# Optimization experiments

Measured on AMD Instinct MI355X. Metric: run time of the kernel, lower is better.

The kernel has to match this reference:

```python
import jax, jax.numpy as jnp
import numpy as np
from jax import lax

DROPOUT_RATE = 0.1  # config['dropout']


def setup_inputs() -> dict:
    key = jax.random.key(0)
    kx, kl, kwi, kwh = jax.random.split(key, 4)
    B, T, D, H = 64, 2048, 256, 256
    datamat = jax.random.normal(kx, (B, T, D), dtype=jnp.float32)
    datalens = jax.random.randint(kl, (B,), 1, T + 1, dtype=jnp.int32)
    # OptimizedLSTMCell params: combined input/hidden kernels, gate order (i, f, g, o)
    s_i = 1.0 / np.sqrt(D)
    s_h = 1.0 / np.sqrt(H)
    Wi = jax.random.uniform(kwi, (D, 4 * H), jnp.float32, -s_i, s_i)
    Wh = jax.random.uniform(kwh, (H, 4 * H), jnp.float32, -s_h, s_h)
    b = jnp.zeros((4 * H,), dtype=jnp.float32)
    return {"datamat": datamat, "Wi": Wi, "Wh": Wh, "b": b, "datalens": datalens}


def _dropout(x, rate):
    # training=True dropout with a fixed key (deterministic reference)
    keep = jax.random.bernoulli(jax.random.key(42), 1.0 - rate, x.shape)
    return jnp.where(keep, x / (1.0 - rate), jnp.zeros_like(x))


def _lstm_forward(x, Wi, Wh, b, datalens):
    # x: [B, T, D]
    B, T, D = x.shape
    H = Wh.shape[0]

    def step(carry, xt):
        c, h = carry
        z = xt @ Wi + h @ Wh + b  # [B, 4H], gate order i, f, g, o
        i, f, g, o = jnp.split(z, 4, axis=-1)
        c_new = jax.nn.sigmoid(f) * c + jax.nn.sigmoid(i) * jnp.tanh(g)
        h_new = jax.nn.sigmoid(o) * jnp.tanh(c_new)
        return (c_new, h_new), (c_new, h_new)

    c0 = jnp.zeros((B, H), dtype=x.dtype)
    h0 = jnp.zeros((B, H), dtype=x.dtype)
    _, (cs, hs) = lax.scan(step, (c0, h0), jnp.swapaxes(x, 0, 1))  # [T, B, H] each
    outputs = jnp.swapaxes(hs, 0, 1)  # [B, T, H]
    # flax nn.RNN with seq_lengths + return_carry: select carry at t = len-1 per batch
    idx = jnp.clip(datalens.astype(jnp.int32) - 1, 0, T - 1)  # [B]
    bidx = jnp.arange(B)
    c_last = cs[idx, bidx]  # [B, H]
    h_last = hs[idx, bidx]  # [B, H]
    return (c_last, h_last), outputs


def reference(datamat, Wi, Wh, b, datalens):
    x = _dropout(datamat, DROPOUT_RATE)
    out_carry, outputs = _lstm_forward(x, Wi, Wh, b, datalens)
    return (out_carry, outputs)
```

## Files before the change

kernel.cpp:

```cpp
#include <hip/hip_runtime.h>


typedef __attribute__((ext_vector_type(8))) short short8;
typedef __attribute__((ext_vector_type(4))) float floatx4;
typedef __attribute__((ext_vector_type(4))) int int4v;
typedef __attribute__((ext_vector_type(4))) unsigned short us4;
typedef __attribute__((ext_vector_type(2))) unsigned int uint2v;

#define LOG2E 1.44269504088896f

__device__ __forceinline__ unsigned short f2bf(float f) {
  unsigned int u = __float_as_uint(f);
  u = u + 0x7fffu + ((u >> 16) & 1u);
  return (unsigned short)(u >> 16);
}
__device__ __forceinline__ float fexp2(float x) { return __builtin_amdgcn_exp2f(x); }
__device__ __forceinline__ float frcp(float x) { return __builtin_amdgcn_rcpf(x); }

__device__ __forceinline__ unsigned int tf_bits(unsigned int x0, unsigned int x1) {
  const unsigned int K0 = 0u, K1 = 42u;
  const unsigned int KX = K0 ^ K1 ^ 0x1BD11BDAu;
  x0 += K0; x1 += K1;
#define TF_R(r) { x0 += x1; x1 = (x1 << (r)) | (x1 >> (32 - (r))); x1 ^= x0; }
  TF_R(13) TF_R(15) TF_R(26) TF_R(6)   x0 += K1; x1 += KX + 1u;
  TF_R(17) TF_R(29) TF_R(16) TF_R(24)  x0 += KX; x1 += K0 + 2u;
  TF_R(13) TF_R(15) TF_R(26) TF_R(6)   x0 += K0; x1 += K1 + 3u;
  TF_R(17) TF_R(29) TF_R(16) TF_R(24)  x0 += K1; x1 += KX + 4u;
  TF_R(13) TF_R(15) TF_R(26) TF_R(6)   x0 += KX; x1 += K0 + 5u;
#undef TF_R
  return x0 ^ x1;
}

__global__ __launch_bounds__(256) void k_dropout(const float* __restrict__ x,
                                                 unsigned short* __restrict__ xd) {
  const unsigned int base = (blockIdx.x * 256u + threadIdx.x) * 4u;
  const float4 xv = *reinterpret_cast<const float4*>(x + base);
  const float xs[4] = {xv.x, xv.y, xv.z, xv.w};
  us4 o;
#pragma unroll
  for (int j = 0; j < 4; ++j) {
    const unsigned int bits = tf_bits(0u, base + (unsigned int)j);
    const float u = __uint_as_float((bits >> 9) | 0x3f800000u) - 1.0f;
    const float v = (u < 0.9f) ? (xs[j] / 0.9f) : 0.0f;
    o[j] = f2bf(v);
  }
  *reinterpret_cast<us4*>(xd + base) = o;
}

__global__ __launch_bounds__(256) void k_pack_wi(const float* __restrict__ wi,
                                                 unsigned short* __restrict__ wit) {
  __shared__ float tile[32][33];
  const int k0 = blockIdx.x * 32, n0 = blockIdx.y * 32;
  const int tx = threadIdx.x & 31, ty = threadIdx.x >> 5;
#pragma unroll
  for (int i = 0; i < 4; ++i)
    tile[ty + i * 8][tx] = wi[(k0 + ty + i * 8) * 1024 + n0 + tx];
  __syncthreads();
#pragma unroll
  for (int i = 0; i < 4; ++i)
    wit[(n0 + ty + i * 8) * 256 + k0 + tx] = f2bf(tile[tx][ty + i * 8]);
}

__global__ __launch_bounds__(256) void k_colscale(const float* __restrict__ wh,
                                                  float* __restrict__ dq,
                                                  float* __restrict__ qs) {
  __shared__ float red[256];
  const int t = threadIdx.x;
  const int n = blockIdx.x * 16 + (t & 15);
  const int kg = t >> 4;
  float m = 0.f;
#pragma unroll
  for (int i = 0; i < 16; ++i)
    m = fmaxf(m, fabsf(wh[(kg * 16 + i) * 1024 + n]));
  red[t] = m;
  __syncthreads();
  if (t < 16) {
    const int nn = blockIdx.x * 16 + t;
    float mm = red[t];
#pragma unroll
    for (int j = 1; j < 16; ++j) mm = fmaxf(mm, red[t + j * 16]);
    const float s = (mm > 0.f) ? mm : 1.f;
    const float gsc[4] = {LOG2E, -LOG2E, 2.f * LOG2E, LOG2E};
    dq[nn] = (s / 16129.0f) * gsc[nn >> 8];
    qs[nn] = 127.0f / s;
  }
}

__global__ __launch_bounds__(256) void k_pack_wh_i8(const float* __restrict__ wh,
                                                    const float* __restrict__ qs,
                                                    signed char* __restrict__ wq) {
  const int tid = blockIdx.x * 256 + threadIdx.x;
  const int j = tid & 15, l = (tid >> 4) & 63, kt = (tid >> 10) & 3, ntg = tid >> 12;
  const int k = kt * 64 + ((l >> 4) << 4) + j;
  const int n = ntg * 16 + (l & 15);
  float v = rintf(wh[k * 1024 + n] * qs[n]);
  v = fminf(fmaxf(v, -127.f), 127.f);
  wq[tid] = (signed char)(int)v;
}

__global__ __launch_bounds__(512, 2) void k_fused(
    const unsigned short* __restrict__ xd, const unsigned short* __restrict__ wit,
    const float* __restrict__ bias, unsigned short* __restrict__ xp,
    const signed char* __restrict__ wq, const float* __restrict__ dq,
    const int* __restrict__ lens, float* __restrict__ out,
    unsigned int* __restrict__ flags) {
  __shared__ __align__(16) unsigned short SH[45056];

  const int tid = threadIdx.x, lane = tid & 63;

  if (blockIdx.x >= 32) {
    const int gb = (int)blockIdx.x - 32;
    const int tc = gb >> 9;
    const int rem = gb & 511;
    const int b = rem >> 3, y = rem & 7;
    const int m0 = b * 2048 + tc * 128;

    const int wv = tid >> 6;
    const int wm = wv >> 2;
    const int wn = wv & 3;
    const int srow = tid >> 2, sseg = tid & 3;
    const unsigned short* gA = xd + (m0 + srow) * 256 + sseg * 8;
    const int nsrc = ((srow >> 5) << 8) + y * 32 + (srow & 31);
    const unsigned short* gB = wit + nsrc * 256 + sseg * 8;
    const int soff = srow * 40 + sseg * 8;

    const floatx4 zero4 = {0.f, 0.f, 0.f, 0.f};
    floatx4 acc[4][2];
#pragma unroll
    for (int i = 0; i < 4; ++i) { acc[i][0] = zero4; acc[i][1] = zero4; }

    short8 ra = *(const short8*)(gA);
    short8 rb = *(const short8*)(gB);
    *(short8*)&SH[soff] = ra;
    *(short8*)&SH[10240 + soff] = rb;
    __syncthreads();

    const int frow = (lane & 15) * 40 + ((lane >> 4) << 3);
#pragma unroll 1
    for (int kt = 0; kt < 8; ++kt) {
      const int boff = (kt & 1) * 5120;
      if (kt < 7) {
        ra = *(const short8*)(gA + (kt + 1) * 32);
        rb = *(const short8*)(gB + (kt + 1) * 32);
      }
      short8 af[4], bfv[2];
#pragma unroll
      for (int mt = 0; mt < 4; ++mt)
        af[mt] = *(const short8*)&SH[boff + (wm * 64 + mt * 16) * 40 + frow];
#pragma unroll
      for (int nt = 0; nt < 2; ++nt)
        bfv[nt] = *(const short8*)&SH[10240 + boff + (wn * 32 + nt * 16) * 40 + frow];
#pragma unroll
      for (int mt = 0; mt < 4; ++mt)
#pragma unroll
        for (int nt = 0; nt < 2; ++nt)
          acc[mt][nt] = __builtin_amdgcn_mfma_f32_16x16x32_bf16(af[mt], bfv[nt], acc[mt][nt], 0, 0, 0);
      if (kt < 7) {
        const int noff = boff ^ 5120;
        *(short8*)&SH[noff + soff] = ra;
        *(short8*)&SH[10240 + noff + soff] = rb;
      }
      __syncthreads();
    }

    const float gsc[4] = {LOG2E, -LOG2E, 2.f * LOG2E, LOG2E};
    const float gv = gsc[wn];
    float bv[2];
#pragma unroll
    for (int nt = 0; nt < 2; ++nt)
      bv[nt] = bias[wn * 256 + y * 32 + nt * 16 + (lane & 15)];

    __syncthreads();
#pragma unroll
    for (int mt = 0; mt < 4; ++mt)
#pragma unroll
      for (int nt = 0; nt < 2; ++nt) {
        const int jj = wn * 32 + nt * 16 + (lane & 15);
#pragma unroll
        for (int q = 0; q < 4; ++q) {
          const int row = wm * 64 + mt * 16 + ((lane >> 4) << 2) + q;
          SH[row * 132 + jj] = f2bf((acc[mt][nt][q] + bv[nt]) * gv);
        }
      }
    __syncthreads();

#pragma unroll
    for (int k = 0; k < 8; ++k) {
      const int pi = k * 512 + tid;
      const int row = pi >> 5, u = pi & 31;
      us4 o = {SH[row * 132 + u], SH[row * 132 + 32 + u],
               SH[row * 132 + 64 + u], SH[row * 132 + 96 + u]};
      const int m = m0 + row;
      unsigned short* p = xp + ((size_t)(m & 2047) * 64 + (m >> 11)) * 1024 +
                          (size_t)(y * 32 + u) * 4;
      const uint2v ov = {(unsigned int)(unsigned short)o[0] | ((unsigned int)(unsigned short)o[1] << 16),
                         (unsigned int)(unsigned short)o[2] | ((unsigned int)(unsigned short)o[3] << 16)};
      asm volatile("global_store_dwordx2 %0, %1, off sc0 sc1"
                   :: "v"(p), "v"(ov) : "memory");
    }

    asm volatile("s_waitcnt vmcnt(0)" ::: "memory");
    __syncthreads();
    if (tid == 0) atomicAdd(&flags[tc], 1u);
    return;
  }

  signed char* As = (signed char*)SH;

  const int v = tid >> 6;
  const int wg = (int)blockIdx.x, b0 = wg * 2;

  const int4v zacc = {0, 0, 0, 0};
  ((int4v*)As)[tid] = zacc;

  int4v w[4][2][4];
#pragma unroll
  for (int g = 0; g < 4; ++g)
#pragma unroll
    for (int p = 0; p < 2; ++p)
#pragma unroll
      for (int kt = 0; kt < 4; ++kt) {
        const int ntg = g * 16 + v * 2 + p;
        w[g][p][kt] = *(const int4v*)(wq + (size_t)(((ntg * 4 + kt) * 64 + lane)) * 16);
      }

  const int r = (lane >> 4) & 1;
  const int ph = lane >> 5;
  const int u = v * 32 + ph * 16 + (lane & 15);

  float dq0 = dq[u], dq1 = dq[256 + u], dq2 = dq[512 + u], dq3 = dq[768 + u];
  const int lenm = lens[b0 + r] - 1;
  float c = 0.f, ckeep = 0.f, hkeep = 0.f;

  const signed char* AsR = As + lane * 16;
  signed char* AsW = As + ((u >> 6) * 1024 + (((u >> 4) & 3) * 16 + r * 4) * 16 + (u & 15));

  const char* xpb = (const char*)xp;
  unsigned int xoff = ((unsigned int)(b0 + r) * 1024u + (unsigned int)u * 4u) * 2u;
  char* outb = (char*)(out + 32768);
  unsigned int ooff = ((unsigned int)(b0 + r) * 524288u + (unsigned int)u) * 4u;

  if (tid == 0) {
    while (__hip_atomic_load(&flags[0], __ATOMIC_ACQUIRE, __HIP_MEMORY_SCOPE_AGENT) < 512u)
      __builtin_amdgcn_s_sleep(8);
  }
  __syncthreads();

  uint2 xc = *(const uint2*)(xpb + xoff);
  xoff += 131072u;

  __syncthreads();

#define GATES(XPAIR, WOFF0, WOFF1)                                              \
  {                                                                             \
    const float xi = __uint_as_float(XPAIR.x << 16);                            \
    const float xf = __uint_as_float(XPAIR.x & 0xffff0000u);                    \
    const float xg = __uint_as_float(XPAIR.y << 16);                            \
    const float xo = __uint_as_float(XPAIR.y & 0xffff0000u);                    \
    const int ai = ph ? acc[0][1][0] : acc[0][0][0];                            \
    const int af_ = ph ? acc[1][1][0] : acc[1][0][0];                           \
    const int ag = ph ? acc[2][1][0] : acc[2][0][0];                            \
    const int ao = ph ? acc[3][1][0] : acc[3][0][0];                            \
    const float zi = fminf(fmaf((float)ai, dq0, xi), 28.85f);                   \
    const float zf = fmaf((float)af_, dq1, xf);                                 \
    const float zg = fminf(fmaf((float)ag, dq2, xg), 57.71f);                   \
    const float zo = fminf(fmaf((float)ao, dq3, xo), 28.85f);                   \
    const float ei = fexp2(zi);                                                 \
    const float e2g = fexp2(zg);                                                \
    const float ef = fexp2(zf);                                                 \
    const float eo = fexp2(zo);                                                 \
    const float p1 = ei * (e2g - 1.f) * frcp((ei + 1.f) * (e2g + 1.f));         \
    const float cn = fmaf(frcp(1.f + ef), c, p1);                               \
    c = cn;                                                                     \
    const float e2c = fexp2(fminf(cn, 15.f) * (2.f * LOG2E));                   \
    const float h = eo * (e2c - 1.f) * frcp((eo + 1.f) * (e2c + 1.f));          \
    const float hm = fmaf(h, 127.f, 12582912.f);                                \
    AsW[WOFF0] = (signed char)__float_as_uint(hm);                              \
    AsW[WOFF1] = (signed char)__float_as_uint(hm);                              \
    *(float*)(outb + ooff) = h;                                                 \
    ooff += 1024u;                                                              \
    if (t_ == lenm) { ckeep = cn; hkeep = h; }                                  \
  }

#define MFMA_BLOCK(O0, O1, O2, O3)                                              \
  int4v acc[4][2];                                                              \
  {                                                                             \
    const int4v a0 = *(const int4v*)(AsR + (O0));                               \
    const int4v a1 = *(const int4v*)(AsR + (O1));                               \
    const int4v a2 = *(const int4v*)(AsR + (O2));                               \
    const int4v a3 = *(const int4v*)(AsR + (O3));                               \
    _Pragma("unroll") for (int g = 0; g < 4; ++g)                               \
    _Pragma("unroll") for (int p = 0; p < 2; ++p) {                             \
      acc[g][p] = __builtin_amdgcn_mfma_i32_16x16x64_i8(a0, w[g][p][0], zacc, 0, 0, 0); \
      acc[g][p] = __builtin_amdgcn_mfma_i32_16x16x64_i8(a1, w[g][p][1], acc[g][p], 0, 0, 0); \
      acc[g][p] = __builtin_amdgcn_mfma_i32_16x16x64_i8(a2, w[g][p][2], acc[g][p], 0, 0, 0); \
      acc[g][p] = __builtin_amdgcn_mfma_i32_16x16x64_i8(a3, w[g][p][3], acc[g][p], 0, 0, 0); \
    }                                                                           \
  }

#pragma unroll 1
  for (int it = 0; it < 1024; ++it) {
    if ((it & 63) == 0) {
      const int ch0 = (it >> 6) + 1;
      const int ch = ch0 < 15 ? ch0 : 15;
      if (tid == 0) {
        while (__hip_atomic_load(&flags[ch], __ATOMIC_ACQUIRE, __HIP_MEMORY_SCOPE_AGENT) < 512u)
          __builtin_amdgcn_s_sleep(8);
      }
      __syncthreads();
    }
    {
      const int t_ = 2 * it;
      const uint2 xn = *(const uint2*)(xpb + xoff);
      xoff += 131072u;
      MFMA_BLOCK(0, 1024, 2048, 3072)
      GATES(xc, 4096, 4224)
      xc = xn;
      __syncthreads();
    }
    {
      const int t_ = 2 * it + 1;
      const uint2 xn = *(const uint2*)(xpb + xoff);
      xoff += 131072u;
      MFMA_BLOCK(4096, 5120, 6144, 7168)
      GATES(xc, 0, 128)
      xc = xn;
      __syncthreads();
    }
  }
#undef GATES
#undef MFMA_BLOCK

  out[(size_t)(b0 + r) * 256 + u] = ckeep;
  out[16384 + (size_t)(b0 + r) * 256 + u] = hkeep;
}

extern "C" void kernel_launch(void* const* d_in, const int* in_sizes, int n_in,
                              void* d_out, int out_size, void* d_ws, size_t ws_size,
                              hipStream_t stream) {
  (void)in_sizes; (void)n_in; (void)out_size; (void)ws_size;
  const float* x = (const float*)d_in[0];
  const float* wi = (const float*)d_in[1];
  const float* wh = (const float*)d_in[2];
  const float* bias = (const float*)d_in[3];
  const int* lens = (const int*)d_in[4];
  float* out = (float*)d_out;

  char* ws = (char*)d_ws;
  unsigned short* xd = (unsigned short*)ws;
  unsigned short* xp = (unsigned short*)(ws + 67108864ull);
  unsigned short* wit = (unsigned short*)(ws + 335544320ull);
  float* dq = (float*)(ws + 336068608ull);
  float* qs = (float*)(ws + 336072704ull);
  signed char* wqb = (signed char*)(ws + 336076800ull);
  unsigned int* flags = (unsigned int*)(ws + 336338944ull);

  hipMemsetAsync(flags, 0, 64, stream);
  k_pack_wi<<<dim3(8, 32), 256, 0, stream>>>(wi, wit);
  k_colscale<<<64, 256, 0, stream>>>(wh, dq, qs);
  k_pack_wh_i8<<<1024, 256, 0, stream>>>(wh, qs, wqb);
  k_dropout<<<32768, 256, 0, stream>>>(x, xd);
  k_fused<<<8224, 512, 0, stream>>>(xd, wit, bias, xp, wqb, dq, lens, out, flags);
}
```

Baseline: 1.505 ms.

## Fuse dropout into input-projection GEMM staging and deepen xp prefetch

Drops the separate dropout kernel and instead computes the threefry dropout mask and bf16 conversion while staging fp32 inputs inside the fused kernel's input-projection GEMM blocks. This avoids writing and re-reading the intermediate bf16 dropped-input buffer. The cost is more ALU work (threefry hashing) in the GEMM load path and twice the global read bytes for fp32 activations. Separately, the recurrent loop now prefetches projected inputs two steps ahead instead of one to hide load latency on the serial critical path.

```diff
diff --git a/kernel.cpp b/kernel.cpp
--- a/kernel.cpp
+++ b/kernel.cpp
@@ -31,20 +31,17 @@
   return x0 ^ x1;
 }
 
-__global__ __launch_bounds__(256) void k_dropout(const float* __restrict__ x,
-                                                 unsigned short* __restrict__ xd) {
-  const unsigned int base = (blockIdx.x * 256u + threadIdx.x) * 4u;
-  const float4 xv = *reinterpret_cast<const float4*>(x + base);
-  const float xs[4] = {xv.x, xv.y, xv.z, xv.w};
-  us4 o;
-#pragma unroll
-  for (int j = 0; j < 4; ++j) {
-    const unsigned int bits = tf_bits(0u, base + (unsigned int)j);
-    const float u = __uint_as_float((bits >> 9) | 0x3f800000u) - 1.0f;
-    const float v = (u < 0.9f) ? (xs[j] / 0.9f) : 0.0f;
-    o[j] = f2bf(v);
-  }
-  *reinterpret_cast<us4*>(xd + base) = o;
+__device__ __forceinline__ short8 stage_drop(const float* __restrict__ g,
+                                             unsigned int n0) {
+  short8 r;
+#pragma unroll
+  for (int j = 0; j < 8; ++j) {
+    const unsigned int bits = tf_bits(0u, n0 + (unsigned int)j);
+    const float uu = __uint_as_float((bits >> 9) | 0x3f800000u) - 1.0f;
+    const float vv = (uu < 0.9f) ? (g[j] / 0.9f) : 0.0f;
+    r[j] = (short)f2bf(vv);
+  }
+  return r;
 }
 
 __global__ __launch_bounds__(256) void k_pack_wi(const float* __restrict__ wi,
@@ -99,7 +96,7 @@
 }
 
 __global__ __launch_bounds__(512, 2) void k_fused(
-    const unsigned short* __restrict__ xd, const unsigned short* __restrict__ wit,
+    const float* __restrict__ x, const unsigned short* __restrict__ wit,
     const float* __restrict__ bias, unsigned short* __restrict__ xp,
     const signed char* __restrict__ wq, const float* __restrict__ dq,
     const int* __restrict__ lens, float* __restrict__ out,
@@ -119,7 +116,8 @@
     const int wm = wv >> 2;
     const int wn = wv & 3;
     const int srow = tid >> 2, sseg = tid & 3;
-    const unsigned short* gA = xd + (m0 + srow) * 256 + sseg * 8;
+    const float* gA = x + (size_t)(m0 + srow) * 256 + sseg * 8;
+    const unsigned int na = (unsigned int)((m0 + srow) * 256 + sseg * 8);
     const int nsrc = ((srow >> 5) << 8) + y * 32 + (srow & 31);
     const unsigned short* gB = wit + nsrc * 256 + sseg * 8;
     const int soff = srow * 40 + sseg * 8;
@@ -129,7 +127,7 @@
 #pragma unroll
     for (int i = 0; i < 4; ++i) { acc[i][0] = zero4; acc[i][1] = zero4; }
 
-    short8 ra = *(const short8*)(gA);
+    short8 ra = stage_drop(gA, na);
     short8 rb = *(const short8*)(gB);
     *(short8*)&SH[soff] = ra;
     *(short8*)&SH[10240 + soff] = rb;
@@ -140,7 +138,7 @@
     for (int kt = 0; kt < 8; ++kt) {
       const int boff = (kt & 1) * 5120;
       if (kt < 7) {
-        ra = *(const short8*)(gA + (kt + 1) * 32);
+        ra = stage_drop(gA + (kt + 1) * 32, na + (unsigned int)(kt + 1) * 32u);
         rb = *(const short8*)(gB + (kt + 1) * 32);
       }
       short8 af[4], bfv[2];
@@ -246,7 +244,9 @@
   }
   __syncthreads();
 
-  uint2 xc = *(const uint2*)(xpb + xoff);
+  uint2 xcur = *(const uint2*)(xpb + xoff);
+  xoff += 131072u;
+  uint2 xnxt = *(const uint2*)(xpb + xoff);
   xoff += 131072u;
 
   __syncthreads();
@@ -311,20 +311,22 @@
     }
     {
       const int t_ = 2 * it;
-      const uint2 xn = *(const uint2*)(xpb + xoff);
+      const uint2 xpre = *(const uint2*)(xpb + xoff);
       xoff += 131072u;
       MFMA_BLOCK(0, 1024, 2048, 3072)
-      GATES(xc, 4096, 4224)
-      xc = xn;
+      GATES(xcur, 4096, 4224)
+      xcur = xnxt;
+      xnxt = xpre;
       __syncthreads();
     }
     {
       const int t_ = 2 * it + 1;
-      const uint2 xn = *(const uint2*)(xpb + xoff);
+      const uint2 xpre = *(const uint2*)(xpb + xoff);
       xoff += 131072u;
       MFMA_BLOCK(4096, 5120, 6144, 7168)
-      GATES(xc, 0, 128)
-      xc = xn;
+      GATES(xcur, 0, 128)
+      xcur = xnxt;
+      xnxt = xpre;
       __syncthreads();
     }
   }
@@ -347,7 +349,6 @@
   float* out = (float*)d_out;
 
   char* ws = (char*)d_ws;
-  unsigned short* xd = (unsigned short*)ws;
   unsigned short* xp = (unsigned short*)(ws + 67108864ull);
   unsigned short* wit = (unsigned short*)(ws + 335544320ull);
   float* dq = (float*)(ws + 336068608ull);
@@ -359,6 +360,5 @@
   k_pack_wi<<<dim3(8, 32), 256, 0, stream>>>(wi, wit);
   k_colscale<<<64, 256, 0, stream>>>(wh, dq, qs);
   k_pack_wh_i8<<<1024, 256, 0, stream>>>(wh, qs, wqb);
-  k_dropout<<<32768, 256, 0, stream>>>(x, xd);
-  k_fused<<<8224, 512, 0, stream>>>(xd, wit, bias, xp, wqb, dq, lens, out, flags);
-}
+  k_fused<<<8224, 512, 0, stream>>>(x, wit, bias, xp, wqb, dq, lens, out, flags);
+}
```

Result: slower. 1.588 ms (+5.4%).
